# Kernel optimization log

Hardware: AMD Instinct MI355X
Metric: run time of the kernel (lower is better)

The kernel has to match this reference:

```python
import jax, jax.numpy as jnp
import numpy as np

STRIDE = 1
PADDING = 1

def setup_inputs() -> dict:
    key = jax.random.key(0)
    k1, k2 = jax.random.split(key)
    x = jax.random.normal(k1, (32, 128, 56, 56), dtype=jnp.float32)
    # kaiming_uniform_(a=sqrt(5)) -> U(-bound, bound), bound = sqrt(6/((1+5)*fan_in)) = 1/sqrt(fan_in)
    fan_in = 128 * 3 * 3
    bound = 1.0 / np.sqrt(fan_in)
    weight = jax.random.uniform(k2, (256, 128, 3, 3), dtype=jnp.float32, minval=-bound, maxval=bound)
    bias = jnp.zeros((256,), dtype=jnp.float32)
    return {"x": x, "weight": weight, "bias": bias}

def reference(x, weight, bias):
    # Dense 2D convolution (cross-correlation, matching torch semantics), NCHW/OIHW.
    out = jax.lax.conv_general_dilated(
        x, weight,
        window_strides=(STRIDE, STRIDE),
        padding=[(PADDING, PADDING), (PADDING, PADDING)],
        dimension_numbers=("NCHW", "OIHW", "NCHW"),
    )
    return out + bias[None, :, None, None]
```

## Files before the change

### kernel.cpp

```cpp
#include <hip/hip_runtime.h>

typedef __bf16 bfvec8 __attribute__((ext_vector_type(8)));
typedef float f32x4 __attribute__((ext_vector_type(4)));
typedef unsigned short u16x8 __attribute__((ext_vector_type(8)));
typedef unsigned int u32;

constexpr int C_IN = 128, Wd = 56, Hd = 56, HW = 3136, K_OUT = 256, N_IMG = 32;
constexpr int KKTOT = 1152;
constexpr int WP = 58;
constexpr size_t XP_ELEMS = (size_t)N_IMG * WP * WP * C_IN;
constexpr size_t XP_BYTES = XP_ELEMS * 2;
constexpr size_t WT_ELEMS = (size_t)9 * 4 * 2 * 128 * 32;
constexpr size_t WS_NEED  = XP_BYTES + WT_ELEMS * 2;

__device__ inline unsigned short f2bf(float f) {
    union { float f; unsigned u; } v; v.f = f;
    unsigned u = v.u;
    u += 0x7fffu + ((u >> 16) & 1u);
    return (unsigned short)(u >> 16);
}

__device__ inline void gld16(const void* g, void* l) {
    __builtin_amdgcn_global_load_lds(
        (const __attribute__((address_space(1))) u32*)g,
        (__attribute__((address_space(3))) u32*)l, 16, 0, 0);
}

__global__ __launch_bounds__(256) void xpose(const float* __restrict__ x,
                                             unsigned short* __restrict__ xp) {
    __shared__ unsigned short T[Wd * C_IN];
    const int nb = blockIdx.x;
    const int n = nb / Hd, h = nb - n * Hd;
    const float* src = x + (size_t)n * C_IN * HW + h * Wd;
    #pragma unroll
    for (int k = 0; k < 7; ++k) {
        int idx = threadIdx.x + k * 256;
        int c = idx / 14, w4 = idx - c * 14;
        const float4 v = *(const float4*)(src + (size_t)c * HW + w4 * 4);
        const int sw = (w4 & 15) * 8;
        T[(w4 * 4 + 0) * C_IN + (c ^ sw)] = f2bf(v.x);
        T[(w4 * 4 + 1) * C_IN + (c ^ sw)] = f2bf(v.y);
        T[(w4 * 4 + 2) * C_IN + (c ^ sw)] = f2bf(v.z);
        T[(w4 * 4 + 3) * C_IN + (c ^ sw)] = f2bf(v.w);
    }
    __syncthreads();
    unsigned short* dst = xp + ((size_t)(n * WP + h + 1) * WP + 1) * C_IN;
    const u16x8* s8 = (const u16x8*)T;
    u16x8* d8 = (u16x8*)dst;
    #pragma unroll
    for (int k = 0; k < 4; ++k) {
        int idx = threadIdx.x + k * 256;
        if (idx < 896) {
            int w = idx >> 4, j8 = idx & 15;
            d8[idx] = s8[w * 16 + (j8 ^ ((w >> 2) & 15))];
        }
    }
}

__global__ __launch_bounds__(256) void wxform(const float* __restrict__ w,
                                              unsigned short* __restrict__ wt) {
    int o = blockIdx.x * 256 + threadIdx.x;
    int kk = o & 31, n = (o >> 5) & 127, nt = (o >> 12) & 1,
        ch = (o >> 13) & 3, rs = o >> 15;
    float v = w[(size_t)(nt * 128 + n) * KKTOT + (ch * 32 + kk) * 9 + rs];
    wt[o] = f2bf(v);
}

__global__ __launch_bounds__(256) void conv_gemm(
    const unsigned short* __restrict__ xp, const unsigned short* __restrict__ wt,
    const float* __restrict__ bias, float* __restrict__ out)
{
    __shared__ __align__(16) unsigned short As[128 * 32];
    __shared__ __align__(16) unsigned short Bs[128 * 32];

    const int tid = threadIdx.x;
    const int bx  = blockIdx.x;
    const int nt  = bx & 1;
    const int mtile = (bx >> 1) * 128;

    const int cg8 = ((tid & 3) ^ ((tid >> 3) & 3)) * 8;

    const unsigned short *gA0, *gA1;
    {
        int mrow = tid >> 2;
        int m = mtile + mrow;
        int ni = m / HW; int hw = m - ni * HW; int h = hw / Wd; int w = hw - h * Wd;
        gA0 = xp + ((size_t)(ni * WP + h + 1) * WP + (w + 1)) * C_IN + cg8;
        m += 64;
        ni = m / HW; hw = m - ni * HW; h = hw / Wd; w = hw - h * Wd;
        gA1 = xp + ((size_t)(ni * WP + h + 1) * WP + (w + 1)) * C_IN + cg8;
    }
    const size_t bbase = (size_t)(tid & 0xFC) * 8 + cg8;

    const int wave = tid >> 6, lane = tid & 63;
    const int wrow = (wave >> 1) * 64, wcol = (wave & 1) * 64;
    const int r16 = lane & 15, quad = lane >> 4;
    const int qsw = (quad ^ ((r16 >> 1) & 3)) * 8;

    const f32x4 zero4 = {0.f, 0.f, 0.f, 0.f};
    f32x4 acc[4][4];
    #pragma unroll
    for (int i = 0; i < 4; ++i)
        #pragma unroll
        for (int j = 0; j < 4; ++j)
            acc[i][j] = zero4;

    for (int step = 0; step < 36; ++step) {
        const int rs = step >> 2, ch = step & 3;
        const int dr = rs / 3 - 1, dc = rs % 3 - 1;
        const int aoff = (dr * WP + dc) * C_IN + ch * 32;
        const size_t boff = (size_t)(((rs * 4 + ch) * 2 + nt) * 4096) + bbase;

        __syncthreads();
        gld16(gA0 + aoff, (void*)(As + tid * 8));
        gld16(gA1 + aoff, (void*)(As + 2048 + tid * 8));
        gld16(wt + boff,        (void*)(Bs + tid * 8));
        gld16(wt + boff + 2048, (void*)(Bs + 2048 + tid * 8));
        __syncthreads();

        bfvec8 af[4], bf[4];
        #pragma unroll
        for (int mi = 0; mi < 4; ++mi)
            af[mi] = *(const bfvec8*)&As[(wrow + mi * 16 + r16) * 32 + qsw];
        #pragma unroll
        for (int ni = 0; ni < 4; ++ni)
            bf[ni] = *(const bfvec8*)&Bs[(wcol + ni * 16 + r16) * 32 + qsw];

        #pragma unroll
        for (int mi = 0; mi < 4; ++mi)
            #pragma unroll
            for (int ni = 0; ni < 4; ++ni)
                acc[mi][ni] = __builtin_amdgcn_mfma_f32_16x16x32_bf16(
                    af[mi], bf[ni], acc[mi][ni], 0, 0, 0);
    }

    const int ntile = nt * 128;
    #pragma unroll
    for (int ni = 0; ni < 4; ++ni) {
        const int k = ntile + wcol + ni * 16 + r16;
        const float bb = bias[k];
        #pragma unroll
        for (int mi = 0; mi < 4; ++mi) {
            const int mb  = mtile + wrow + mi * 16 + quad * 4;
            const int ne  = mb / HW;
            const int hwe = mb - ne * HW;
            f32x4 v;
            #pragma unroll
            for (int i = 0; i < 4; ++i) v[i] = acc[mi][ni][i] + bb;
            *(f32x4*)(out + ((size_t)ne * K_OUT + k) * HW + hwe) = v;
        }
    }
}

extern "C" void kernel_launch(void* const* d_in, const int* in_sizes, int n_in,
                              void* d_out, int out_size, void* d_ws, size_t ws_size,
                              hipStream_t stream) {
    const float* x    = (const float*)d_in[0];
    const float* wgt  = (const float*)d_in[1];
    const float* bias = (const float*)d_in[2];
    float* out = (float*)d_out;

    unsigned short* xp = (unsigned short*)d_ws;
    unsigned short* wt = (unsigned short*)((char*)d_ws + XP_BYTES);

    hipMemsetAsync(d_ws, 0, XP_BYTES, stream);
    xpose<<<dim3(N_IMG * Hd), dim3(256), 0, stream>>>(x, xp);
    wxform<<<dim3((int)(WT_ELEMS / 256)), dim3(256), 0, stream>>>(wgt, wt);
    conv_gemm<<<dim3(1568), dim3(256), 0, stream>>>(xp, wt, bias, out);
}
```

Baseline: 231.0 us.

## Fuse prep kernels, zero only halo, double-buffer LDS, widen GEMM tile to 128x256

The memset, transpose and weight-transform launches are merged into one prep kernel that zeroes only the padding border instead of the whole padded buffer. The conv GEMM now computes a full 256-channel N tile per block (784 blocks), with each wave holding a 64x128 accumulator, which removes the duplicated A-tile loads across the two N halves. LDS is double-buffered so the next step's global-to-LDS loads are issued before the current tile is computed, cutting one barrier per step. Register pressure roughly doubles (128 accumulator floats per lane) and LDS grows to about 48KB, which may lower occupancy.

```diff
diff --git a/kernel.cpp b/kernel.cpp
--- a/kernel.cpp
+++ b/kernel.cpp
@@ -10,8 +10,7 @@
 constexpr int WP = 58;
 constexpr size_t XP_ELEMS = (size_t)N_IMG * WP * WP * C_IN;
 constexpr size_t XP_BYTES = XP_ELEMS * 2;
-constexpr size_t WT_ELEMS = (size_t)9 * 4 * 2 * 128 * 32;
-constexpr size_t WS_NEED  = XP_BYTES + WT_ELEMS * 2;
+constexpr size_t WT_ELEMS = (size_t)9 * 4 * 256 * 32;
 
 __device__ inline unsigned short f2bf(float f) {
     union { float f; unsigned u; } v; v.f = f;
@@ -26,65 +25,81 @@
         (__attribute__((address_space(3))) u32*)l, 16, 0, 0);
 }
 
-__global__ __launch_bounds__(256) void xpose(const float* __restrict__ x,
-                                             unsigned short* __restrict__ xp) {
-    __shared__ unsigned short T[Wd * C_IN];
-    const int nb = blockIdx.x;
-    const int n = nb / Hd, h = nb - n * Hd;
-    const float* src = x + (size_t)n * C_IN * HW + h * Wd;
-    #pragma unroll
-    for (int k = 0; k < 7; ++k) {
-        int idx = threadIdx.x + k * 256;
-        int c = idx / 14, w4 = idx - c * 14;
-        const float4 v = *(const float4*)(src + (size_t)c * HW + w4 * 4);
-        const int sw = (w4 & 15) * 8;
-        T[(w4 * 4 + 0) * C_IN + (c ^ sw)] = f2bf(v.x);
-        T[(w4 * 4 + 1) * C_IN + (c ^ sw)] = f2bf(v.y);
-        T[(w4 * 4 + 2) * C_IN + (c ^ sw)] = f2bf(v.z);
-        T[(w4 * 4 + 3) * C_IN + (c ^ sw)] = f2bf(v.w);
-    }
-    __syncthreads();
-    unsigned short* dst = xp + ((size_t)(n * WP + h + 1) * WP + 1) * C_IN;
-    const u16x8* s8 = (const u16x8*)T;
-    u16x8* d8 = (u16x8*)dst;
-    #pragma unroll
-    for (int k = 0; k < 4; ++k) {
-        int idx = threadIdx.x + k * 256;
-        if (idx < 896) {
-            int w = idx >> 4, j8 = idx & 15;
-            d8[idx] = s8[w * 16 + (j8 ^ ((w >> 2) & 15))];
+__global__ __launch_bounds__(256) void prep(const float* __restrict__ x,
+                                            const float* __restrict__ w,
+                                            unsigned short* __restrict__ xp,
+                                            unsigned short* __restrict__ wt) {
+    const int bx = blockIdx.x, tid = threadIdx.x;
+    if (bx < 1792) {
+        __shared__ unsigned short T[Wd * C_IN];
+        const int n = bx / Hd, h = bx - n * Hd;
+        const float* src = x + (size_t)n * C_IN * HW + h * Wd;
+        #pragma unroll
+        for (int k = 0; k < 7; ++k) {
+            int idx = tid + k * 256;
+            int c = idx / 14, w4 = idx - c * 14;
+            const float4 v = *(const float4*)(src + (size_t)c * HW + w4 * 4);
+            const int sw = (w4 & 15) * 8;
+            T[(w4 * 4 + 0) * C_IN + (c ^ sw)] = f2bf(v.x);
+            T[(w4 * 4 + 1) * C_IN + (c ^ sw)] = f2bf(v.y);
+            T[(w4 * 4 + 2) * C_IN + (c ^ sw)] = f2bf(v.z);
+            T[(w4 * 4 + 3) * C_IN + (c ^ sw)] = f2bf(v.w);
+        }
+        __syncthreads();
+        unsigned short* dst = xp + ((size_t)(n * WP + h + 1) * WP + 1) * C_IN;
+        const u16x8* s8 = (const u16x8*)T;
+        u16x8* d8 = (u16x8*)dst;
+        #pragma unroll
+        for (int k = 0; k < 4; ++k) {
+            int idx = tid + k * 256;
+            if (idx < 896) {
+                int ww = idx >> 4, j8 = idx & 15;
+                d8[idx] = s8[ww * 16 + (j8 ^ ((ww >> 2) & 15))];
+            }
+        }
+    } else if (bx < 1824) {
+        const int n = bx - 1792;
+        u16x8 z = {0, 0, 0, 0, 0, 0, 0, 0};
+        u16x8* base = (u16x8*)(xp + (size_t)n * WP * WP * C_IN);
+        #pragma unroll
+        for (int it = 0; it < 15; ++it) {
+            int v = tid + it * 256;
+            if (v < 928) base[v] = z;
+            else if (v < 1856) base[52896 + (v - 928)] = z;
+            else if (v < 3648) {
+                int u = v - 1856, seg = u >> 4, j = u & 15;
+                int h = 1 + (seg >> 1), side = seg & 1;
+                base[(h * WP + side * 57) * 16 + j] = z;
+            }
+        }
+    } else {
+        const int o0 = (bx - 1824) * 4608 + tid;
+        #pragma unroll
+        for (int j = 0; j < 18; ++j) {
+            int o = o0 + j * 256;
+            int kk = o & 31, n = (o >> 5) & 255, r2 = o >> 13;
+            int ch = r2 & 3, rs = r2 >> 2;
+            wt[o] = f2bf(w[(size_t)n * KKTOT + (ch * 32 + kk) * 9 + rs]);
         }
     }
-}
-
-__global__ __launch_bounds__(256) void wxform(const float* __restrict__ w,
-                                              unsigned short* __restrict__ wt) {
-    int o = blockIdx.x * 256 + threadIdx.x;
-    int kk = o & 31, n = (o >> 5) & 127, nt = (o >> 12) & 1,
-        ch = (o >> 13) & 3, rs = o >> 15;
-    float v = w[(size_t)(nt * 128 + n) * KKTOT + (ch * 32 + kk) * 9 + rs];
-    wt[o] = f2bf(v);
 }
 
 __global__ __launch_bounds__(256) void conv_gemm(
     const unsigned short* __restrict__ xp, const unsigned short* __restrict__ wt,
     const float* __restrict__ bias, float* __restrict__ out)
 {
-    __shared__ __align__(16) unsigned short As[128 * 32];
-    __shared__ __align__(16) unsigned short Bs[128 * 32];
+    __shared__ __align__(16) unsigned short As[2][128 * 32];
+    __shared__ __align__(16) unsigned short Bs[2][256 * 32];
 
     const int tid = threadIdx.x;
-    const int bx  = blockIdx.x;
-    const int nt  = bx & 1;
-    const int mtile = (bx >> 1) * 128;
+    const int mtile = blockIdx.x * 128;
 
     const int cg8 = ((tid & 3) ^ ((tid >> 3) & 3)) * 8;
 
     const unsigned short *gA0, *gA1;
     {
-        int mrow = tid >> 2;
-        int m = mtile + mrow;
-        int ni = m / HW; int hw = m - ni * HW; int h = hw / Wd; int w = hw - h * Wd;
+        int m = mtile + (tid >> 2);
+        int ni = m / HW, hw = m - ni * HW, h = hw / Wd, w = hw - h * Wd;
         gA0 = xp + ((size_t)(ni * WP + h + 1) * WP + (w + 1)) * C_IN + cg8;
         m += 64;
         ni = m / HW; hw = m - ni * HW; h = hw / Wd; w = hw - h * Wd;
@@ -93,51 +108,60 @@
     const size_t bbase = (size_t)(tid & 0xFC) * 8 + cg8;
 
     const int wave = tid >> 6, lane = tid & 63;
-    const int wrow = (wave >> 1) * 64, wcol = (wave & 1) * 64;
+    const int wrow = (wave & 1) * 64;
+    const int wcol = (wave >> 1) * 128;
     const int r16 = lane & 15, quad = lane >> 4;
     const int qsw = (quad ^ ((r16 >> 1) & 3)) * 8;
 
     const f32x4 zero4 = {0.f, 0.f, 0.f, 0.f};
-    f32x4 acc[4][4];
+    f32x4 acc[4][8];
     #pragma unroll
     for (int i = 0; i < 4; ++i)
         #pragma unroll
-        for (int j = 0; j < 4; ++j)
+        for (int j = 0; j < 8; ++j)
             acc[i][j] = zero4;
 
-    for (int step = 0; step < 36; ++step) {
+    auto stage = [&](int step, int b) {
         const int rs = step >> 2, ch = step & 3;
         const int dr = rs / 3 - 1, dc = rs % 3 - 1;
         const int aoff = (dr * WP + dc) * C_IN + ch * 32;
-        const size_t boff = (size_t)(((rs * 4 + ch) * 2 + nt) * 4096) + bbase;
+        const size_t boff = (size_t)((rs * 4 + ch) * 8192) + bbase;
+        unsigned short* a = &As[b][0] + tid * 8;
+        unsigned short* bl = &Bs[b][0] + tid * 8;
+        gld16(gA0 + aoff, a);
+        gld16(gA1 + aoff, a + 2048);
+        gld16(wt + boff,        bl);
+        gld16(wt + boff + 2048, bl + 2048);
+        gld16(wt + boff + 4096, bl + 4096);
+        gld16(wt + boff + 6144, bl + 6144);
+    };
 
+    stage(0, 0);
+    int cur = 0;
+    for (int step = 0; step < 36; ++step) {
         __syncthreads();
-        gld16(gA0 + aoff, (void*)(As + tid * 8));
-        gld16(gA1 + aoff, (void*)(As + 2048 + tid * 8));
-        gld16(wt + boff,        (void*)(Bs + tid * 8));
-        gld16(wt + boff + 2048, (void*)(Bs + 2048 + tid * 8));
-        __syncthreads();
+        if (step < 35) stage(step + 1, cur ^ 1);
 
-        bfvec8 af[4], bf[4];
+        bfvec8 af[4], bf[8];
         #pragma unroll
         for (int mi = 0; mi < 4; ++mi)
-            af[mi] = *(const bfvec8*)&As[(wrow + mi * 16 + r16) * 32 + qsw];
+            af[mi] = *(const bfvec8*)&As[cur][(wrow + mi * 16 + r16) * 32 + qsw];
         #pragma unroll
-        for (int ni = 0; ni < 4; ++ni)
-            bf[ni] = *(const bfvec8*)&Bs[(wcol + ni * 16 + r16) * 32 + qsw];
+        for (int ni = 0; ni < 8; ++ni)
+            bf[ni] = *(const bfvec8*)&Bs[cur][(wcol + ni * 16 + r16) * 32 + qsw];
 
         #pragma unroll
         for (int mi = 0; mi < 4; ++mi)
             #pragma unroll
-            for (int ni = 0; ni < 4; ++ni)
+            for (int ni = 0; ni < 8; ++ni)
                 acc[mi][ni] = __builtin_amdgcn_mfma_f32_16x16x32_bf16(
                     af[mi], bf[ni], acc[mi][ni], 0, 0, 0);
+        cur ^= 1;
     }
 
-    const int ntile = nt * 128;
     #pragma unroll
-    for (int ni = 0; ni < 4; ++ni) {
-        const int k = ntile + wcol + ni * 16 + r16;
+    for (int ni = 0; ni < 8; ++ni) {
+        const int k = wcol + ni * 16 + r16;
         const float bb = bias[k];
         #pragma unroll
         for (int mi = 0; mi < 4; ++mi) {
@@ -163,8 +187,6 @@
     unsigned short* xp = (unsigned short*)d_ws;
     unsigned short* wt = (unsigned short*)((char*)d_ws + XP_BYTES);
 
-    hipMemsetAsync(d_ws, 0, XP_BYTES, stream);
-    xpose<<<dim3(N_IMG * Hd), dim3(256), 0, stream>>>(x, xp);
-    wxform<<<dim3((int)(WT_ELEMS / 256)), dim3(256), 0, stream>>>(wgt, wt);
-    conv_gemm<<<dim3(1568), dim3(256), 0, stream>>>(xp, wt, bias, out);
+    prep<<<dim3(1888), dim3(256), 0, stream>>>(x, wgt, xp, wt);
+    conv_gemm<<<dim3(784), dim3(256), 0, stream>>>(xp, wt, bias, out);
 }
```

After: 258.5 us. 11.9% more time.
